# Performance work log

Measured on AMD Instinct MI355X. Metric: run time of the kernel, lower is better.

The kernel has to match this reference:

```python
import jax, jax.numpy as jnp
import numpy as np

N = 10000      # nodes
E = 160000     # edges
G = 64         # graphs
NODE_IN = 115
EDGE_IN = 14
H = 256        # hidden
UH = 64        # EdgeUpdate inner hidden
DEPTH = 5
BN_EPS = 1e-5


def setup_inputs() -> dict:
    key = jax.random.key(0)
    ks = jax.random.split(key, 32)
    p = lambda k, shp: (jax.random.normal(k, shp, dtype=jnp.float32) * 0.05)
    inp = {
        "x": jax.random.normal(ks[0], (N, NODE_IN), dtype=jnp.float32),
        "edge_index": jax.random.randint(ks[1], (2, E), 0, N, dtype=jnp.int64) if jax.config.jax_enable_x64 else jax.random.randint(ks[1], (2, E), 0, N).astype(jnp.int32),
        "edge_attr": jax.random.normal(ks[2], (E, EDGE_IN), dtype=jnp.float32),
        "batch": jnp.sort(jax.random.randint(ks[3], (N,), 0, G)).astype(jnp.int32),
        # projections
        "xp_w": p(ks[4], (NODE_IN, H)), "xp_b": jnp.zeros((H,), jnp.float32),
        "ep_w": p(ks[5], (EDGE_IN, H)), "ep_b": jnp.zeros((H,), jnp.float32),
        # EdgeUpdate MLPs (stacked over depth): Linear(3H -> UH) -> ReLU -> Linear(UH -> H)
        "upd_w1": p(ks[6], (DEPTH, 3 * H, UH)), "upd_b1": jnp.zeros((DEPTH, UH), jnp.float32),
        "upd_w2": p(ks[7], (DEPTH, UH, H)),     "upd_b2": jnp.zeros((DEPTH, H), jnp.float32),
        # GINEConv nn MLPs: Linear(H->H) -> ReLU -> Linear(H->H)
        "conv_w1": p(ks[8], (DEPTH, H, H)), "conv_b1": jnp.zeros((DEPTH, H), jnp.float32),
        "conv_w2": p(ks[9], (DEPTH, H, H)), "conv_b2": jnp.zeros((DEPTH, H), jnp.float32),
        # BatchNorm (eval mode: running stats)
        "bn_g": jnp.ones((DEPTH, H), jnp.float32), "bn_b": jnp.zeros((DEPTH, H), jnp.float32),
        "bn_m": jnp.zeros((DEPTH, H), jnp.float32), "bn_v": jnp.ones((DEPTH, H), jnp.float32),
        # readout
        "ro_w": p(ks[10], (H, H)), "ro_b": jnp.zeros((H,), jnp.float32),
    }
    return inp


def reference(x, edge_index, edge_attr, batch, xp_w, xp_b, ep_w, ep_b,
              upd_w1, upd_b1, upd_w2, upd_b2,
              conv_w1, conv_b1, conv_w2, conv_b2,
              bn_g, bn_b, bn_m, bn_v, ro_w, ro_b):
    src, dst = edge_index[0], edge_index[1]
    x = x @ xp_w + xp_b                       # [N, H]
    e = edge_attr @ ep_w + ep_b               # [E, H]
    for i in range(DEPTH):
        # EdgeUpdate: e = e + MLP([x[src], x[dst], e])
        inp = jnp.concatenate([x[src], x[dst], e], axis=-1)          # [E, 3H]
        h = jax.nn.relu(inp @ upd_w1[i] + upd_b1[i])
        e = e + h @ upd_w2[i] + upd_b2[i]
        # GINEConv (eps=0, edge_dim==hidden -> no edge lin):
        # x_new = mlp(x + sum_{(src->dst)} relu(x[src] + e))
        msg = jax.nn.relu(x[src] + e)                                 # [E, H]
        agg = jax.ops.segment_sum(msg, dst, num_segments=N)           # [N, H]
        z = x + agg
        z = jax.nn.relu(z @ conv_w1[i] + conv_b1[i]) @ conv_w2[i] + conv_b2[i]
        # BatchNorm1d (eval: running stats)
        z = (z - bn_m[i]) * jax.lax.rsqrt(bn_v[i] + BN_EPS) * bn_g[i] + bn_b[i]
        x = x + jax.nn.relu(z)
        # dropout is identity in eval mode
    # global_mean_pool over graphs
    counts = jax.ops.segment_sum(jnp.ones((N,), x.dtype), batch, num_segments=G)
    g = jax.ops.segment_sum(x, batch, num_segments=G) / jnp.maximum(counts, 1.0)[:, None]
    return jax.nn.relu(g @ ro_w + ro_b)       # [G, H]
```

## Files before the change

### kernel.cpp

```cpp
#include <hip/hip_runtime.h>

typedef unsigned short ushort_t;
typedef __attribute__((ext_vector_type(4))) float f32x4;
typedef __attribute__((ext_vector_type(8))) short bf16x8;

constexpr int NN = 10000;
constexpr int NE = 160000;
constexpr int NG = 64;
constexpr int NODE_IN_D = 115;
constexpr int EDGE_IN_D = 14;
constexpr int H = 256;
constexpr int UH = 64;
constexpr int DEPTH_D = 5;
constexpr float BN_EPS_F = 1e-5f;

__device__ __forceinline__ float b2fs(ushort_t u) {
  union { unsigned i; float f; } v; v.i = ((unsigned)u) << 16; return v.f;
}
__device__ __forceinline__ ushort_t f2b(float f) {
  union { float f; unsigned i; } v; v.f = f;
  unsigned x = v.i;
  unsigned r = (x + 0x7fffu + ((x >> 16) & 1u)) >> 16;
  return (ushort_t)r;
}

__global__ __launch_bounds__(256) void k_hist(const int* __restrict__ dst,
                                              int* __restrict__ deg)
{
  int j = blockIdx.x * 256 + threadIdx.x;
  if (j < NE) atomicAdd(&deg[dst[j]], 1);
}

__global__ __launch_bounds__(256) void k_scan(const int* __restrict__ deg,
    int* __restrict__ row_ptr, int* __restrict__ cursor)
{
  __shared__ int part[256];
  const int t = threadIdx.x;
  const int base = t * 40;
  int s = 0;
  for (int i = 0; i < 40; ++i) {
    int idx = base + i;
    if (idx < NN) s += deg[idx];
  }
  part[t] = s;
  __syncthreads();
  for (int off = 1; off < 256; off <<= 1) {
    int v = (t >= off) ? part[t - off] : 0;
    __syncthreads();
    part[t] += v;
    __syncthreads();
  }
  int run = (t > 0) ? part[t - 1] : 0;
  for (int i = 0; i < 40; ++i) {
    int idx = base + i;
    if (idx < NN) {
      row_ptr[idx] = run;
      cursor[idx]  = run;
      run += deg[idx];
    }
  }
  if (t == 255) row_ptr[NN] = NE;
}

__global__ __launch_bounds__(256) void k_scatter(const int* __restrict__ src,
    const int* __restrict__ dst, int* __restrict__ cursor,
    int* __restrict__ perm, int* __restrict__ src_p, int* __restrict__ dst_p)
{
  int j = blockIdx.x * 256 + threadIdx.x;
  if (j < NE) {
    int d = dst[j];
    int pos = atomicAdd(&cursor[d], 1);
    perm[pos] = j;
    src_p[pos] = src[j];
    dst_p[pos] = d;
  }
}

__global__ __launch_bounds__(256) void k_proj_edge(const float* __restrict__ ea,
    const int* __restrict__ perm,
    const float* __restrict__ w, const float* __restrict__ b,
    ushort_t* __restrict__ e_p)
{
  __shared__ float as[16][EDGE_IN_D];
  __shared__ int pj[16];
  const int t = threadIdx.x;
  const int row0 = blockIdx.x * 16;
  if (t < 16) pj[t] = perm[row0 + t];
  __syncthreads();
  if (t < 16 * EDGE_IN_D) {
    int r = t / EDGE_IN_D, c = t - r * EDGE_IN_D;
    as[r][c] = ea[(size_t)pj[r] * EDGE_IN_D + c];
  }
  __syncthreads();
  float acc[16];
#pragma unroll
  for (int m = 0; m < 16; ++m) acc[m] = 0.f;
  for (int k = 0; k < EDGE_IN_D; ++k) {
    float wv = w[(size_t)k * H + t];
#pragma unroll
    for (int m = 0; m < 16; ++m) acc[m] += as[m][k] * wv;
  }
  const float bv = b[t];
  for (int m = 0; m < 16; ++m)
    e_p[(size_t)(row0 + m) * H + t] = f2b(acc[m] + bv);
}

__global__ __launch_bounds__(256) void k_pack_all(
    const float* __restrict__ uw1, const float* __restrict__ uw2,
    const float* __restrict__ cw1, const float* __restrict__ cw2,
    const float* __restrict__ xp_w,
    ushort_t* __restrict__ wcP, ushort_t* __restrict__ w2P,
    ushort_t* __restrict__ c1P, ushort_t* __restrict__ c2P,
    ushort_t* __restrict__ pabP, ushort_t* __restrict__ xpP)
{
  int od = blockIdx.x * 256 + threadIdx.x;
  if (od >= DEPTH_D * 24576) {
    int r = od - DEPTH_D * 24576;
    if (r >= 4096) return;
    int lane = r & 63; int nk = r >> 6;
    int ks = nk & 3, nt = nk >> 2;
    int kbase = ks * 32 + (lane >> 4) * 8;
    int n = nt * 16 + (lane & 15);
    ushort_t v[8];
#pragma unroll
    for (int j = 0; j < 8; ++j) {
      int k = kbase + j;
      v[j] = (k < NODE_IN_D) ? f2b(xp_w[(size_t)k * H + n]) : (ushort_t)0;
    }
    uint4 o;
    o.x = (unsigned)v[0] | ((unsigned)v[1] << 16);
    o.y = (unsigned)v[2] | ((unsigned)v[3] << 16);
    o.z = (unsigned)v[4] | ((unsigned)v[5] << 16);
    o.w = (unsigned)v[6] | ((unsigned)v[7] << 16);
    *(uint4*)(xpP + (size_t)r * 8) = o;
    return;
  }
  int depth = od / 24576;
  int r = od - depth * 24576;
  const float* w1d = uw1 + (size_t)depth * 768 * 64;
  const float* W = nullptr; ushort_t* out = nullptr;
  int N = 0, KS = 8; bool pab = false;
  if (r < 2048)       { W = w1d + 512 * 64; out = wcP + (size_t)depth * 2048 * 8; N = 64; KS = 8; }
  else if (r < 4096)  { r -= 2048;  W = uw2 + (size_t)depth * 64 * 256;  out = w2P + (size_t)depth * 2048 * 8; N = 256; KS = 2; }
  else if (r < 12288) { r -= 4096;  W = cw1 + (size_t)depth * 256 * 256; out = c1P + (size_t)depth * 8192 * 8; N = 256; KS = 8; }
  else if (r < 20480) { r -= 12288; W = cw2 + (size_t)depth * 256 * 256; out = c2P + (size_t)depth * 8192 * 8; N = 256; KS = 8; }
  else                { r -= 20480; out = pabP + (size_t)depth * 4096 * 8; N = 128; KS = 8; pab = true; }
  int lane = r & 63; int nk = r >> 6;
  int ks = nk % KS, nt = nk / KS;
  int kbase = ks * 32 + (lane >> 4) * 8;
  int n = nt * 16 + (lane & 15);
  ushort_t v[8];
#pragma unroll
  for (int j = 0; j < 8; ++j) {
    int k = kbase + j;
    float xv;
    if (!pab) xv = W[(size_t)k * N + n];
    else      xv = (n < 64) ? w1d[(size_t)k * 64 + n]
                            : w1d[(size_t)(256 + k) * 64 + (n - 64)];
    v[j] = f2b(xv);
  }
  uint4 o;
  o.x = (unsigned)v[0] | ((unsigned)v[1] << 16);
  o.y = (unsigned)v[2] | ((unsigned)v[3] << 16);
  o.z = (unsigned)v[4] | ((unsigned)v[5] << 16);
  o.w = (unsigned)v[6] | ((unsigned)v[7] << 16);
  *(uint4*)(out + (size_t)r * 8) = o;
}

__global__ __launch_bounds__(256) void k_projm(const float* __restrict__ x,
    const ushort_t* __restrict__ xpP, const float* __restrict__ xpb,
    const ushort_t* __restrict__ pabP0,
    float* __restrict__ xb, float* __restrict__ Pab)
{
  __shared__ __align__(16) ushort_t sa[2 * 32 * 128];
  __shared__ __align__(16) ushort_t sx[2 * 32 * 256];
  const int t = threadIdx.x, l = t & 63, w = t >> 6;
  const int row0 = blockIdx.x * 32;
#pragma unroll
  for (int it = 0; it < 16; ++it) {
    int idx = t + it * 256;
    int row = idx >> 7, c = idx & 127;
    int grow = row0 + row;
    float v = (grow < NN && c < NODE_IN_D) ? x[(size_t)grow * NODE_IN_D + c] : 0.f;
    ushort_t h = f2b(v);
    ushort_t lo = f2b(v - b2fs(h));
    int sch = (row * 16 + ((c >> 3) ^ (row & 7))) * 8 + (c & 7);
    sa[sch] = h; sa[4096 + sch] = lo;
  }
  __syncthreads();
  const int mt = w & 1, ntb = (w >> 1) * 8;
  const int lrow = l & 15, lhi = l >> 4;
  const int arow = mt * 16 + lrow, sw = arow & 7;
  f32x4 acc[8];
#pragma unroll
  for (int n = 0; n < 8; ++n) acc[n] = (f32x4){0.f, 0.f, 0.f, 0.f};
#pragma unroll
  for (int ks = 0; ks < 4; ++ks) {
    int sch = (arow * 16 + ((ks * 4 + lhi) ^ sw)) * 8;
    bf16x8 ah = *(const bf16x8*)&sa[sch];
    bf16x8 al = *(const bf16x8*)&sa[4096 + sch];
#pragma unroll
    for (int n = 0; n < 8; ++n) {
      bf16x8 bb = *(const bf16x8*)(xpP + (size_t)(((ntb + n) * 4 + ks) * 64 + l) * 8);
      acc[n] = __builtin_amdgcn_mfma_f32_16x16x32_bf16(ah, bb, acc[n], 0, 0, 0);
      acc[n] = __builtin_amdgcn_mfma_f32_16x16x32_bf16(al, bb, acc[n], 0, 0, 0);
    }
  }
#pragma unroll
  for (int n = 0; n < 8; ++n) {
    int col = (ntb + n) * 16 + lrow;
    float bv = xpb[col];
#pragma unroll
    for (int r = 0; r < 4; ++r) {
      int row = mt * 16 + lhi * 4 + r;
      int grow = row0 + row;
      float v = acc[n][r] + bv;
      if (grow < NN) xb[(size_t)grow * H + col] = v;
      ushort_t h = f2b(v);
      ushort_t lo = f2b(v - b2fs(h));
      int sch = (row * 32 + ((col >> 3) ^ (row & 7))) * 8 + (col & 7);
      sx[sch] = h; sx[8192 + sch] = lo;
    }
  }
  __syncthreads();
  const int ntb2 = (w >> 1) * 4;
  f32x4 pacc[4];
#pragma unroll
  for (int n = 0; n < 4; ++n) pacc[n] = (f32x4){0.f, 0.f, 0.f, 0.f};
#pragma unroll
  for (int ks = 0; ks < 8; ++ks) {
    int sch = (arow * 32 + ((ks * 4 + lhi) ^ sw)) * 8;
    bf16x8 ah = *(const bf16x8*)&sx[sch];
    bf16x8 al = *(const bf16x8*)&sx[8192 + sch];
#pragma unroll
    for (int n = 0; n < 4; ++n) {
      bf16x8 bb = *(const bf16x8*)(pabP0 + (size_t)(((ntb2 + n) * 8 + ks) * 64 + l) * 8);
      pacc[n] = __builtin_amdgcn_mfma_f32_16x16x32_bf16(ah, bb, pacc[n], 0, 0, 0);
      pacc[n] = __builtin_amdgcn_mfma_f32_16x16x32_bf16(al, bb, pacc[n], 0, 0, 0);
    }
  }
#pragma unroll
  for (int n = 0; n < 4; ++n) {
    int col = (ntb2 + n) * 16 + lrow;
#pragma unroll
    for (int r = 0; r < 4; ++r) {
      int row = mt * 16 + lhi * 4 + r;
      int grow = row0 + row;
      if (grow < NN) Pab[(size_t)grow * 128 + col] = pacc[n][r];
    }
  }
}

__global__ __launch_bounds__(256) void k_edge_mfma(
    const float* __restrict__ Pab,
    const int* __restrict__ src_p, const int* __restrict__ dst_p,
    const ushort_t* __restrict__ wcP, const float* __restrict__ b1,
    const ushort_t* __restrict__ w2P, const float* __restrict__ b2,
    ushort_t* __restrict__ e_p)
{
  __shared__ __align__(16) ushort_t es[64 * 256];
  __shared__ __align__(16) ushort_t hsm[64 * 64];
  __shared__ int sid[64], did[64];
  const int t = threadIdx.x;
  const int l = t & 63;
  const int w = t >> 6;
  const int e0 = blockIdx.x * 64;
  if (t < 64) { sid[t] = src_p[e0 + t]; did[t] = dst_p[e0 + t]; }
#pragma unroll
  for (int it = 0; it < 8; ++it) {
    int idx = t + it * 256;
    int row = idx >> 5, ch = idx & 31;
    uint4 v = *(const uint4*)(e_p + (size_t)(e0 + row) * H + ch * 8);
    *(uint4*)&es[(row * 32 + (ch ^ (row & 7))) * 8] = v;
  }
  __syncthreads();

  const int rw = w * 16;
  const int lrow = l & 15, lhi = l >> 4;

  bf16x8 af[8];
  {
    int arow = rw + lrow;
    int sw = arow & 7;
#pragma unroll
    for (int ks = 0; ks < 8; ++ks)
      af[ks] = *(const bf16x8*)&es[(arow * 32 + ((ks * 4 + lhi) ^ sw)) * 8];
  }
  f32x4 acc[4];
#pragma unroll
  for (int nt = 0; nt < 4; ++nt) {
    f32x4 a = {0.f, 0.f, 0.f, 0.f};
#pragma unroll
    for (int ks = 0; ks < 8; ++ks) {
      bf16x8 bb = *(const bf16x8*)(wcP + (size_t)((nt * 8 + ks) * 64 + l) * 8);
      a = __builtin_amdgcn_mfma_f32_16x16x32_bf16(af[ks], bb, a, 0, 0, 0);
    }
    acc[nt] = a;
  }
#pragma unroll
  for (int nt = 0; nt < 4; ++nt) {
    int col = nt * 16 + lrow;
    float bv = b1[col];
#pragma unroll
    for (int r = 0; r < 4; ++r) {
      int row = rw + lhi * 4 + r;
      float v = acc[nt][r] + Pab[(size_t)sid[row] * 128 + col]
                           + Pab[(size_t)did[row] * 128 + 64 + col] + bv;
      hsm[row * 64 + (col ^ ((row & 7) << 3))] = f2b(fmaxf(v, 0.f));
    }
  }
  __syncthreads();

  bf16x8 ag[2];
  {
    int arow = rw + lrow;
    int sw = arow & 7;
#pragma unroll
    for (int ks = 0; ks < 2; ++ks)
      ag[ks] = *(const bf16x8*)&hsm[arow * 64 + (((ks * 4 + lhi) ^ sw)) * 8];
  }
#pragma unroll
  for (int nt = 0; nt < 16; ++nt) {
    int col = nt * 16 + lrow;
    float bv = b2[col];
    f32x4 a;
#pragma unroll
    for (int r = 0; r < 4; ++r) {
      int row = rw + lhi * 4 + r;
      a[r] = b2fs(es[row * 256 + (col ^ ((row & 7) << 3))]) + bv;
    }
    bf16x8 bb0 = *(const bf16x8*)(w2P + (size_t)((nt * 2 + 0) * 64 + l) * 8);
    bf16x8 bb1 = *(const bf16x8*)(w2P + (size_t)((nt * 2 + 1) * 64 + l) * 8);
    a = __builtin_amdgcn_mfma_f32_16x16x32_bf16(ag[0], bb0, a, 0, 0, 0);
    a = __builtin_amdgcn_mfma_f32_16x16x32_bf16(ag[1], bb1, a, 0, 0, 0);
#pragma unroll
    for (int r = 0; r < 4; ++r) {
      int row = rw + lhi * 4 + r;
      es[row * 256 + (col ^ ((row & 7) << 3))] = f2b(a[r]);
    }
  }
  __syncthreads();
#pragma unroll
  for (int it = 0; it < 8; ++it) {
    int idx = t + it * 256;
    int row = idx >> 5, ch = idx & 31;
    uint4 v = *(const uint4*)&es[(row * 32 + (ch ^ (row & 7))) * 8];
    *(uint4*)(e_p + (size_t)(e0 + row) * H + ch * 8) = v;
  }
}

__global__ __launch_bounds__(256) void k_agg(
    const ushort_t* __restrict__ e_p, const float* __restrict__ xb,
    const int* __restrict__ src_p, const int* __restrict__ row_ptr,
    float* __restrict__ agg)
{
  const int t = threadIdx.x;
  const int n = blockIdx.x * 4 + (t >> 6);
  const int c0 = (t & 63) * 4;
  const int beg = row_ptr[n], end = row_ptr[n + 1];
  float4 acc = make_float4(0.f, 0.f, 0.f, 0.f);
  for (int j = beg; j < end; ++j) {
    ushort4 ev = *(const ushort4*)(e_p + (size_t)j * H + c0);
    const float4 xv = *(const float4*)(xb + (size_t)src_p[j] * H + c0);
    acc.x += fmaxf(xv.x + b2fs(ev.x), 0.f);
    acc.y += fmaxf(xv.y + b2fs(ev.y), 0.f);
    acc.z += fmaxf(xv.z + b2fs(ev.z), 0.f);
    acc.w += fmaxf(xv.w + b2fs(ev.w), 0.f);
  }
  *(float4*)(agg + (size_t)n * H + c0) = acc;
}

__global__ __launch_bounds__(256) void k_conv1m(const float* __restrict__ xb,
    const float* __restrict__ agg, const ushort_t* __restrict__ wP,
    const float* __restrict__ b, float* __restrict__ t1)
{
  __shared__ __align__(16) ushort_t sm[2 * 16 * 256];
  __shared__ __align__(16) float outs[16 * 256];
  const int t = threadIdx.x, l = t & 63, w = t >> 6;
  const int row0 = blockIdx.x * 16;
#pragma unroll
  for (int it = 0; it < 2; ++it) {
    int idx = t + it * 256;
    int row = idx >> 5, ch = idx & 31;
    int grow = row0 + row;
    float4 p = *(const float4*)(xb + (size_t)grow * H + ch * 8);
    float4 q = *(const float4*)(xb + (size_t)grow * H + ch * 8 + 4);
    float4 g = *(const float4*)(agg + (size_t)grow * H + ch * 8);
    float4 h4 = *(const float4*)(agg + (size_t)grow * H + ch * 8 + 4);
    float v[8] = {p.x + g.x, p.y + g.y, p.z + g.z, p.w + g.w,
                  q.x + h4.x, q.y + h4.y, q.z + h4.z, q.w + h4.w};
    ushort_t h8[8], l8[8];
#pragma unroll
    for (int j = 0; j < 8; ++j) { h8[j] = f2b(v[j]); l8[j] = f2b(v[j] - b2fs(h8[j])); }
    uint4 hh, ll;
    hh.x = (unsigned)h8[0] | ((unsigned)h8[1] << 16);
    hh.y = (unsigned)h8[2] | ((unsigned)h8[3] << 16);
    hh.z = (unsigned)h8[4] | ((unsigned)h8[5] << 16);
    hh.w = (unsigned)h8[6] | ((unsigned)h8[7] << 16);
    ll.x = (unsigned)l8[0] | ((unsigned)l8[1] << 16);
    ll.y = (unsigned)l8[2] | ((unsigned)l8[3] << 16);
    ll.z = (unsigned)l8[4] | ((unsigned)l8[5] << 16);
    ll.w = (unsigned)l8[6] | ((unsigned)l8[7] << 16);
    int sch = (row * 32 + (ch ^ (row & 7))) * 8;
    *(uint4*)&sm[sch] = hh;
    *(uint4*)&sm[4096 + sch] = ll;
  }
  __syncthreads();
  const int lrow = l & 15, lhi = l >> 4;
  const int arow = lrow, sw = arow & 7;
  const int ntb = w * 4;
  f32x4 acc[4];
#pragma unroll
  for (int n = 0; n < 4; ++n) acc[n] = (f32x4){0.f, 0.f, 0.f, 0.f};
#pragma unroll
  for (int ks = 0; ks < 8; ++ks) {
    int sch = (arow * 32 + ((ks * 4 + lhi) ^ sw)) * 8;
    bf16x8 ah = *(const bf16x8*)&sm[sch];
    bf16x8 al = *(const bf16x8*)&sm[4096 + sch];
#pragma unroll
    for (int n = 0; n < 4; ++n) {
      bf16x8 bb = *(const bf16x8*)(wP + (size_t)(((ntb + n) * 8 + ks) * 64 + l) * 8);
      acc[n] = __builtin_amdgcn_mfma_f32_16x16x32_bf16(ah, bb, acc[n], 0, 0, 0);
      acc[n] = __builtin_amdgcn_mfma_f32_16x16x32_bf16(al, bb, acc[n], 0, 0, 0);
    }
  }
#pragma unroll
  for (int n = 0; n < 4; ++n) {
    int col = (ntb + n) * 16 + lrow;
    float bv = b[col];
#pragma unroll
    for (int r = 0; r < 4; ++r)
      outs[(lhi * 4 + r) * 256 + col] = fmaxf(acc[n][r] + bv, 0.f);
  }
  __syncthreads();
#pragma unroll
  for (int it = 0; it < 4; ++it) {
    int idx = t + it * 256;
    int row = idx >> 6, c4 = idx & 63;
    *(float4*)(t1 + (size_t)(row0 + row) * H + c4 * 4) = *(float4*)&outs[row * 256 + c4 * 4];
  }
}

__global__ __launch_bounds__(256) void k_conv2m(const float* __restrict__ t1,
    const ushort_t* __restrict__ wP, const float* __restrict__ cb,
    const float* __restrict__ bng, const float* __restrict__ bnb,
    const float* __restrict__ bnm, const float* __restrict__ bnv,
    float* __restrict__ xb, int do_pab,
    const ushort_t* __restrict__ pabPn, float* __restrict__ Pab)
{
  __shared__ __align__(16) ushort_t sm[2 * 16 * 256];
  __shared__ __align__(16) float outs[16 * 256];
  __shared__ __align__(16) ushort_t sx[2 * 16 * 256];
  const int t = threadIdx.x, l = t & 63, w = t >> 6;
  const int row0 = blockIdx.x * 16;
#pragma unroll
  for (int it = 0; it < 2; ++it) {
    int idx = t + it * 256;
    int row = idx >> 5, ch = idx & 31;
    int grow = row0 + row;
    float4 p = *(const float4*)(t1 + (size_t)grow * H + ch * 8);
    float4 q = *(const float4*)(t1 + (size_t)grow * H + ch * 8 + 4);
    float v[8] = {p.x, p.y, p.z, p.w, q.x, q.y, q.z, q.w};
    ushort_t h8[8], l8[8];
#pragma unroll
    for (int j = 0; j < 8; ++j) { h8[j] = f2b(v[j]); l8[j] = f2b(v[j] - b2fs(h8[j])); }
    uint4 hh, ll;
    hh.x = (unsigned)h8[0] | ((unsigned)h8[1] << 16);
    hh.y = (unsigned)h8[2] | ((unsigned)h8[3] << 16);
    hh.z = (unsigned)h8[4] | ((unsigned)h8[5] << 16);
    hh.w = (unsigned)h8[6] | ((unsigned)h8[7] << 16);
    ll.x = (unsigned)l8[0] | ((unsigned)l8[1] << 16);
    ll.y = (unsigned)l8[2] | ((unsigned)l8[3] << 16);
    ll.z = (unsigned)l8[4] | ((unsigned)l8[5] << 16);
    ll.w = (unsigned)l8[6] | ((unsigned)l8[7] << 16);
    int sch = (row * 32 + (ch ^ (row & 7))) * 8;
    *(uint4*)&sm[sch] = hh;
    *(uint4*)&sm[4096 + sch] = ll;
  }
  __syncthreads();
  const int lrow = l & 15, lhi = l >> 4;
  const int arow = lrow, sw = arow & 7;
  const int ntb = w * 4;
  f32x4 acc[4];
#pragma unroll
  for (int n = 0; n < 4; ++n) acc[n] = (f32x4){0.f, 0.f, 0.f, 0.f};
#pragma unroll
  for (int ks = 0; ks < 8; ++ks) {
    int sch = (arow * 32 + ((ks * 4 + lhi) ^ sw)) * 8;
    bf16x8 ah = *(const bf16x8*)&sm[sch];
    bf16x8 al = *(const bf16x8*)&sm[4096 + sch];
#pragma unroll
    for (int n = 0; n < 4; ++n) {
      bf16x8 bb = *(const bf16x8*)(wP + (size_t)(((ntb + n) * 8 + ks) * 64 + l) * 8);
      acc[n] = __builtin_amdgcn_mfma_f32_16x16x32_bf16(ah, bb, acc[n], 0, 0, 0);
      acc[n] = __builtin_amdgcn_mfma_f32_16x16x32_bf16(al, bb, acc[n], 0, 0, 0);
    }
  }
#pragma unroll
  for (int n = 0; n < 4; ++n) {
    int col = (ntb + n) * 16 + lrow;
    float bv = cb[col];
#pragma unroll
    for (int r = 0; r < 4; ++r)
      outs[(lhi * 4 + r) * 256 + col] = acc[n][r] + bv;
  }
  __syncthreads();
#pragma unroll
  for (int it = 0; it < 4; ++it) {
    int idx = t + it * 256;
    int row = idx >> 6, c4 = idx & 63;
    int grow = row0 + row;
    int c0 = c4 * 4;
    float4 z = *(float4*)&outs[row * 256 + c0];
    float4 g4 = *(const float4*)(bng + c0);
    float4 b4 = *(const float4*)(bnb + c0);
    float4 m4 = *(const float4*)(bnm + c0);
    float4 v4 = *(const float4*)(bnv + c0);
    float4 xv = *(const float4*)(xb + (size_t)grow * H + c0);
    xv.x += fmaxf((z.x - m4.x) * rsqrtf(v4.x + BN_EPS_F) * g4.x + b4.x, 0.f);
    xv.y += fmaxf((z.y - m4.y) * rsqrtf(v4.y + BN_EPS_F) * g4.y + b4.y, 0.f);
    xv.z += fmaxf((z.z - m4.z) * rsqrtf(v4.z + BN_EPS_F) * g4.z + b4.z, 0.f);
    xv.w += fmaxf((z.w - m4.w) * rsqrtf(v4.w + BN_EPS_F) * g4.w + b4.w, 0.f);
    *(float4*)(xb + (size_t)grow * H + c0) = xv;
    if (do_pab) {
      ushort4 hh, ll;
      float vv[4] = {xv.x, xv.y, xv.z, xv.w};
      ushort_t h8[4], l8[4];
#pragma unroll
      for (int j = 0; j < 4; ++j) { h8[j] = f2b(vv[j]); l8[j] = f2b(vv[j] - b2fs(h8[j])); }
      hh.x = h8[0]; hh.y = h8[1]; hh.z = h8[2]; hh.w = h8[3];
      ll.x = l8[0]; ll.y = l8[1]; ll.z = l8[2]; ll.w = l8[3];
      int sch = (row * 32 + ((c0 >> 3) ^ (row & 7))) * 8 + (c0 & 7);
      *(ushort4*)&sx[sch] = hh;
      *(ushort4*)&sx[4096 + sch] = ll;
    }
  }
  if (!do_pab) return;
  __syncthreads();
  const int ntb2 = w * 2;
  f32x4 pacc[2];
#pragma unroll
  for (int n = 0; n < 2; ++n) pacc[n] = (f32x4){0.f, 0.f, 0.f, 0.f};
#pragma unroll
  for (int ks = 0; ks < 8; ++ks) {
    int sch = (arow * 32 + ((ks * 4 + lhi) ^ sw)) * 8;
    bf16x8 ah = *(const bf16x8*)&sx[sch];
    bf16x8 al = *(const bf16x8*)&sx[4096 + sch];
#pragma unroll
    for (int n = 0; n < 2; ++n) {
      bf16x8 bb = *(const bf16x8*)(pabPn + (size_t)(((ntb2 + n) * 8 + ks) * 64 + l) * 8);
      pacc[n] = __builtin_amdgcn_mfma_f32_16x16x32_bf16(ah, bb, pacc[n], 0, 0, 0);
      pacc[n] = __builtin_amdgcn_mfma_f32_16x16x32_bf16(al, bb, pacc[n], 0, 0, 0);
    }
  }
#pragma unroll
  for (int n = 0; n < 2; ++n) {
    int col = (ntb2 + n) * 16 + lrow;
#pragma unroll
    for (int r = 0; r < 4; ++r)
      Pab[(size_t)(row0 + lhi * 4 + r) * 128 + col] = pacc[n][r];
  }
}

__global__ void k_count2(const int* __restrict__ batch, float* __restrict__ gcnt)
{
  int g = threadIdx.x;
  int lo = 0, hi = NN;
  while (lo < hi) { int m = (lo + hi) >> 1; if (batch[m] < g) lo = m + 1; else hi = m; }
  int s = lo;
  lo = 0; hi = NN;
  while (lo < hi) { int m = (lo + hi) >> 1; if (batch[m] <= g) lo = m + 1; else hi = m; }
  gcnt[g] = (float)(lo - s);
}

__global__ __launch_bounds__(256) void k_pool(const float* __restrict__ xb,
    const int* __restrict__ batch, float* __restrict__ gsum)
{
  const int t = threadIdx.x;
  const int row0 = blockIdx.x * 32;
  const int c0 = (t & 63) * 4;
  const int rb = (t >> 6) * 8;
  float4 sum = make_float4(0.f, 0.f, 0.f, 0.f);
  int curg = -1;
#pragma unroll
  for (int j = 0; j < 8; ++j) {
    int row = row0 + rb + j;
    if (row < NN) {
      int g = batch[row];
      if (g != curg) {
        if (curg >= 0) {
          float* gp = gsum + (size_t)curg * H + c0;
          atomicAdd(gp + 0, sum.x); atomicAdd(gp + 1, sum.y);
          atomicAdd(gp + 2, sum.z); atomicAdd(gp + 3, sum.w);
        }
        curg = g;
        sum = make_float4(0.f, 0.f, 0.f, 0.f);
      }
      float4 v = *(const float4*)(xb + (size_t)row * H + c0);
      sum.x += v.x; sum.y += v.y; sum.z += v.z; sum.w += v.w;
    }
  }
  if (curg >= 0) {
    float* gp = gsum + (size_t)curg * H + c0;
    atomicAdd(gp + 0, sum.x); atomicAdd(gp + 1, sum.y);
    atomicAdd(gp + 2, sum.z); atomicAdd(gp + 3, sum.w);
  }
}

__global__ __launch_bounds__(256) void k_readout(const float* __restrict__ gsum,
    const float* __restrict__ gcnt, const float* __restrict__ w,
    const float* __restrict__ b, float* __restrict__ out)
{
  __shared__ float gs[H];
  const int g = blockIdx.x;
  const int t = threadIdx.x;
  float cnt = fmaxf(gcnt[g], 1.0f);
  gs[t] = gsum[(size_t)g * H + t] / cnt;
  __syncthreads();
  float acc = 0.f;
  for (int k = 0; k < H; ++k) acc += gs[k] * w[(size_t)k * H + t];
  out[(size_t)g * H + t] = fmaxf(acc + b[t], 0.f);
}

extern "C" void kernel_launch(void* const* d_in, const int* in_sizes, int n_in,
                              void* d_out, int out_size, void* d_ws, size_t ws_size,
                              hipStream_t stream) {
  (void)in_sizes; (void)n_in; (void)out_size; (void)ws_size;
  const float* x    = (const float*)d_in[0];
  const int*   ei   = (const int*)d_in[1];
  const float* ea   = (const float*)d_in[2];
  const int*   batch= (const int*)d_in[3];
  const float* xp_w = (const float*)d_in[4];
  const float* xp_b = (const float*)d_in[5];
  const float* ep_w = (const float*)d_in[6];
  const float* ep_b = (const float*)d_in[7];
  const float* uw1  = (const float*)d_in[8];
  const float* ub1  = (const float*)d_in[9];
  const float* uw2  = (const float*)d_in[10];
  const float* ub2  = (const float*)d_in[11];
  const float* cw1  = (const float*)d_in[12];
  const float* cb1  = (const float*)d_in[13];
  const float* cw2  = (const float*)d_in[14];
  const float* cb2  = (const float*)d_in[15];
  const float* bng  = (const float*)d_in[16];
  const float* bnb  = (const float*)d_in[17];
  const float* bnm  = (const float*)d_in[18];
  const float* bnv  = (const float*)d_in[19];
  const float* ro_w = (const float*)d_in[20];
  const float* ro_b = (const float*)d_in[21];
  float* out = (float*)d_out;

  char* ws = (char*)d_ws;
  float* xb   = (float*)ws;                  ws += (size_t)NN * H * 4;
  float* agg  = (float*)ws;                  ws += (size_t)NN * H * 4;
  float* t1   = (float*)ws;                  ws += (size_t)NN * H * 4;
  float* Pab  = (float*)ws;                  ws += (size_t)NN * 128 * 4;
  float* gsum = (float*)ws;                  ws += (size_t)NG * H * 4;
  float* gcnt = (float*)ws;                  ws += 256;
  ushort_t* e_p = (ushort_t*)ws;             ws += (size_t)NE * H * 2;
  int* deg    = (int*)ws;                    ws += (size_t)NN * 4;
  int* row_ptr= (int*)ws;                    ws += (size_t)(NN + 8) * 4;
  int* cursor = (int*)ws;                    ws += (size_t)NN * 4;
  int* perm   = (int*)ws;                    ws += (size_t)NE * 4;
  int* src_p  = (int*)ws;                    ws += (size_t)NE * 4;
  int* dst_p  = (int*)ws;                    ws += (size_t)NE * 4;
  ushort_t* wcP = (ushort_t*)ws;             ws += (size_t)DEPTH_D * 2048 * 8 * 2;
  ushort_t* w2P = (ushort_t*)ws;             ws += (size_t)DEPTH_D * 2048 * 8 * 2;
  ushort_t* c1P = (ushort_t*)ws;             ws += (size_t)DEPTH_D * 8192 * 8 * 2;
  ushort_t* c2P = (ushort_t*)ws;             ws += (size_t)DEPTH_D * 8192 * 8 * 2;
  ushort_t* pabP= (ushort_t*)ws;             ws += (size_t)DEPTH_D * 4096 * 8 * 2;
  ushort_t* xpP = (ushort_t*)ws;             ws += (size_t)4096 * 8 * 2;

  const int* src = ei;
  const int* dst = ei + NE;
  const int EB = NE / 256;

  hipMemsetAsync(deg, 0, (size_t)NN * 4, stream);
  k_hist<<<EB, 256, 0, stream>>>(dst, deg);
  k_scan<<<1, 256, 0, stream>>>(deg, row_ptr, cursor);
  k_scatter<<<EB, 256, 0, stream>>>(src, dst, cursor, perm, src_p, dst_p);
  k_pack_all<<<496, 256, 0, stream>>>(uw1, uw2, cw1, cw2, xp_w,
                                      wcP, w2P, c1P, c2P, pabP, xpP);
  k_projm<<<313, 256, 0, stream>>>(x, xpP, xp_b, pabP, xb, Pab);
  k_proj_edge<<<NE / 16, 256, 0, stream>>>(ea, perm, ep_w, ep_b, e_p);

  for (int i = 0; i < DEPTH_D; ++i) {
    k_edge_mfma<<<NE / 64, 256, 0, stream>>>(
        Pab, src_p, dst_p,
        wcP + (size_t)i * 2048 * 8, ub1 + (size_t)i * UH,
        w2P + (size_t)i * 2048 * 8, ub2 + (size_t)i * H,
        e_p);
    k_agg<<<NN / 4, 256, 0, stream>>>(e_p, xb, src_p, row_ptr, agg);
    k_conv1m<<<NN / 16, 256, 0, stream>>>(xb, agg, c1P + (size_t)i * 8192 * 8,
                                          cb1 + (size_t)i * H, t1);
    int do_pab = (i < DEPTH_D - 1) ? 1 : 0;
    k_conv2m<<<NN / 16, 256, 0, stream>>>(t1, c2P + (size_t)i * 8192 * 8,
                                          cb2 + (size_t)i * H,
                                          bng + (size_t)i * H, bnb + (size_t)i * H,
                                          bnm + (size_t)i * H, bnv + (size_t)i * H,
                                          xb, do_pab,
                                          pabP + (size_t)(i + 1 < DEPTH_D ? i + 1 : 0) * 4096 * 8,
                                          Pab);
  }

  hipMemsetAsync(gsum, 0, (size_t)NG * H * 4, stream);
  k_count2<<<1, 64, 0, stream>>>(batch, gcnt);
  k_pool<<<(NN + 31) / 32, 256, 0, stream>>>(xb, batch, gsum);
  k_readout<<<NG, 256, 0, stream>>>(gsum, gcnt, ro_w, ro_b, out);
}
```

Measured before the change: 662.6 us.

## Fuse edge aggregation into edge-update kernel and merge both conv MLP kernels

The dst-sorted segment sum moves into the edge MLP kernel. Each wave accumulates relu(x[src]+e) over runs of equal dst in its 16 edges and flushes to agg with fp32 atomics, so the separate k_agg pass no longer re-reads the updated edge tensor. The two GINE MLP GEMM kernels become one, keeping the hidden activation in shared memory as hi/lo bf16 instead of a global t1 buffer. The final layer also skips writing the edge tensor back. The cost is a per-layer memset of agg, atomic contention, non-deterministic summation order, and higher shared-memory use in the fused conv kernel.

```diff
diff --git a/kernel.cpp b/kernel.cpp
--- a/kernel.cpp
+++ b/kernel.cpp
@@ -256,7 +256,8 @@
     const int* __restrict__ src_p, const int* __restrict__ dst_p,
     const ushort_t* __restrict__ wcP, const float* __restrict__ b1,
     const ushort_t* __restrict__ w2P, const float* __restrict__ b2,
-    ushort_t* __restrict__ e_p)
+    ushort_t* __restrict__ e_p,
+    const float* __restrict__ xb, float* __restrict__ agg, int write_e)
 {
   __shared__ __align__(16) ushort_t es[64 * 256];
   __shared__ __align__(16) ushort_t hsm[64 * 64];
@@ -340,41 +341,56 @@
     }
   }
   __syncthreads();
-#pragma unroll
-  for (int it = 0; it < 8; ++it) {
-    int idx = t + it * 256;
-    int row = idx >> 5, ch = idx & 31;
-    uint4 v = *(const uint4*)&es[(row * 32 + (ch ^ (row & 7))) * 8];
-    *(uint4*)(e_p + (size_t)(e0 + row) * H + ch * 8) = v;
-  }
-}
-
-__global__ __launch_bounds__(256) void k_agg(
-    const ushort_t* __restrict__ e_p, const float* __restrict__ xb,
-    const int* __restrict__ src_p, const int* __restrict__ row_ptr,
-    float* __restrict__ agg)
-{
-  const int t = threadIdx.x;
-  const int n = blockIdx.x * 4 + (t >> 6);
-  const int c0 = (t & 63) * 4;
-  const int beg = row_ptr[n], end = row_ptr[n + 1];
-  float4 acc = make_float4(0.f, 0.f, 0.f, 0.f);
-  for (int j = beg; j < end; ++j) {
-    ushort4 ev = *(const ushort4*)(e_p + (size_t)j * H + c0);
-    const float4 xv = *(const float4*)(xb + (size_t)src_p[j] * H + c0);
-    acc.x += fmaxf(xv.x + b2fs(ev.x), 0.f);
-    acc.y += fmaxf(xv.y + b2fs(ev.y), 0.f);
-    acc.z += fmaxf(xv.z + b2fs(ev.z), 0.f);
-    acc.w += fmaxf(xv.w + b2fs(ev.w), 0.f);
-  }
-  *(float4*)(agg + (size_t)n * H + c0) = acc;
-}
-
-__global__ __launch_bounds__(256) void k_conv1m(const float* __restrict__ xb,
-    const float* __restrict__ agg, const ushort_t* __restrict__ wP,
-    const float* __restrict__ b, float* __restrict__ t1)
+
+  if (write_e) {
+#pragma unroll
+    for (int it = 0; it < 8; ++it) {
+      int idx = t + it * 256;
+      int row = idx >> 5, ch = idx & 31;
+      uint4 v = *(const uint4*)&es[(row * 32 + (ch ^ (row & 7))) * 8];
+      *(uint4*)(e_p + (size_t)(e0 + row) * H + ch * 8) = v;
+    }
+  }
+
+  {
+    const int c0 = l * 4;
+    float4 acc4 = make_float4(0.f, 0.f, 0.f, 0.f);
+    int cur = did[rw];
+#pragma unroll
+    for (int r = 0; r < 16; ++r) {
+      int row = rw + r;
+      int d = did[row];
+      if (d != cur) {
+        float* gp = agg + (size_t)cur * H + c0;
+        atomicAdd(gp + 0, acc4.x); atomicAdd(gp + 1, acc4.y);
+        atomicAdd(gp + 2, acc4.z); atomicAdd(gp + 3, acc4.w);
+        acc4 = make_float4(0.f, 0.f, 0.f, 0.f);
+        cur = d;
+      }
+      ushort4 ev = *(const ushort4*)&es[row * 256 + (c0 ^ ((row & 7) << 3))];
+      float4 xv = *(const float4*)(xb + (size_t)sid[row] * H + c0);
+      acc4.x += fmaxf(xv.x + b2fs(ev.x), 0.f);
+      acc4.y += fmaxf(xv.y + b2fs(ev.y), 0.f);
+      acc4.z += fmaxf(xv.z + b2fs(ev.z), 0.f);
+      acc4.w += fmaxf(xv.w + b2fs(ev.w), 0.f);
+    }
+    float* gp = agg + (size_t)cur * H + c0;
+    atomicAdd(gp + 0, acc4.x); atomicAdd(gp + 1, acc4.y);
+    atomicAdd(gp + 2, acc4.z); atomicAdd(gp + 3, acc4.w);
+  }
+}
+
+__global__ __launch_bounds__(256) void k_convm(
+    const float* __restrict__ agg,
+    const ushort_t* __restrict__ w1P, const float* __restrict__ b1v,
+    const ushort_t* __restrict__ w2P, const float* __restrict__ cb2v,
+    const float* __restrict__ bng, const float* __restrict__ bnb,
+    const float* __restrict__ bnm, const float* __restrict__ bnv,
+    float* __restrict__ xb, int do_pab,
+    const ushort_t* __restrict__ pabPn, float* __restrict__ Pab)
 {
   __shared__ __align__(16) ushort_t sm[2 * 16 * 256];
+  __shared__ __align__(16) ushort_t st1[2 * 16 * 256];
   __shared__ __align__(16) float outs[16 * 256];
   const int t = threadIdx.x, l = t & 63, w = t >> 6;
   const int row0 = blockIdx.x * 16;
@@ -419,7 +435,7 @@
     bf16x8 al = *(const bf16x8*)&sm[4096 + sch];
 #pragma unroll
     for (int n = 0; n < 4; ++n) {
-      bf16x8 bb = *(const bf16x8*)(wP + (size_t)(((ntb + n) * 8 + ks) * 64 + l) * 8);
+      bf16x8 bb = *(const bf16x8*)(w1P + (size_t)(((ntb + n) * 8 + ks) * 64 + l) * 8);
       acc[n] = __builtin_amdgcn_mfma_f32_16x16x32_bf16(ah, bb, acc[n], 0, 0, 0);
       acc[n] = __builtin_amdgcn_mfma_f32_16x16x32_bf16(al, bb, acc[n], 0, 0, 0);
     }
@@ -427,82 +443,40 @@
 #pragma unroll
   for (int n = 0; n < 4; ++n) {
     int col = (ntb + n) * 16 + lrow;
-    float bv = b[col];
-#pragma unroll
-    for (int r = 0; r < 4; ++r)
-      outs[(lhi * 4 + r) * 256 + col] = fmaxf(acc[n][r] + bv, 0.f);
-  }
-  __syncthreads();
-#pragma unroll
-  for (int it = 0; it < 4; ++it) {
-    int idx = t + it * 256;
-    int row = idx >> 6, c4 = idx & 63;
-    *(float4*)(t1 + (size_t)(row0 + row) * H + c4 * 4) = *(float4*)&outs[row * 256 + c4 * 4];
-  }
-}
-
-__global__ __launch_bounds__(256) void k_conv2m(const float* __restrict__ t1,
-    const ushort_t* __restrict__ wP, const float* __restrict__ cb,
-    const float* __restrict__ bng, const float* __restrict__ bnb,
-    const float* __restrict__ bnm, const float* __restrict__ bnv,
-    float* __restrict__ xb, int do_pab,
-    const ushort_t* __restrict__ pabPn, float* __restrict__ Pab)
-{
-  __shared__ __align__(16) ushort_t sm[2 * 16 * 256];
-  __shared__ __align__(16) float outs[16 * 256];
-  __shared__ __align__(16) ushort_t sx[2 * 16 * 256];
-  const int t = threadIdx.x, l = t & 63, w = t >> 6;
-  const int row0 = blockIdx.x * 16;
-#pragma unroll
-  for (int it = 0; it < 2; ++it) {
-    int idx = t + it * 256;
-    int row = idx >> 5, ch = idx & 31;
-    int grow = row0 + row;
-    float4 p = *(const float4*)(t1 + (size_t)grow * H + ch * 8);
-    float4 q = *(const float4*)(t1 + (size_t)grow * H + ch * 8 + 4);
-    float v[8] = {p.x, p.y, p.z, p.w, q.x, q.y, q.z, q.w};
-    ushort_t h8[8], l8[8];
-#pragma unroll
-    for (int j = 0; j < 8; ++j) { h8[j] = f2b(v[j]); l8[j] = f2b(v[j] - b2fs(h8[j])); }
-    uint4 hh, ll;
-    hh.x = (unsigned)h8[0] | ((unsigned)h8[1] << 16);
-    hh.y = (unsigned)h8[2] | ((unsigned)h8[3] << 16);
-    hh.z = (unsigned)h8[4] | ((unsigned)h8[5] << 16);
-    hh.w = (unsigned)h8[6] | ((unsigned)h8[7] << 16);
-    ll.x = (unsigned)l8[0] | ((unsigned)l8[1] << 16);
-    ll.y = (unsigned)l8[2] | ((unsigned)l8[3] << 16);
-    ll.z = (unsigned)l8[4] | ((unsigned)l8[5] << 16);
-    ll.w = (unsigned)l8[6] | ((unsigned)l8[7] << 16);
-    int sch = (row * 32 + (ch ^ (row & 7))) * 8;
-    *(uint4*)&sm[sch] = hh;
-    *(uint4*)&sm[4096 + sch] = ll;
-  }
-  __syncthreads();
-  const int lrow = l & 15, lhi = l >> 4;
-  const int arow = lrow, sw = arow & 7;
-  const int ntb = w * 4;
-  f32x4 acc[4];
-#pragma unroll
-  for (int n = 0; n < 4; ++n) acc[n] = (f32x4){0.f, 0.f, 0.f, 0.f};
+    float bv = b1v[col];
+#pragma unroll
+    for (int r = 0; r < 4; ++r) {
+      int row = lhi * 4 + r;
+      float v = fmaxf(acc[n][r] + bv, 0.f);
+      ushort_t h = f2b(v);
+      ushort_t lo = f2b(v - b2fs(h));
+      int sch = (row * 32 + ((col >> 3) ^ (row & 7))) * 8 + (col & 7);
+      st1[sch] = h; st1[4096 + sch] = lo;
+    }
+  }
+  __syncthreads();
+  f32x4 acc2[4];
+#pragma unroll
+  for (int n = 0; n < 4; ++n) acc2[n] = (f32x4){0.f, 0.f, 0.f, 0.f};
 #pragma unroll
   for (int ks = 0; ks < 8; ++ks) {
     int sch = (arow * 32 + ((ks * 4 + lhi) ^ sw)) * 8;
-    bf16x8 ah = *(const bf16x8*)&sm[sch];
-    bf16x8 al = *(const bf16x8*)&sm[4096 + sch];
+    bf16x8 ah = *(const bf16x8*)&st1[sch];
+    bf16x8 al = *(const bf16x8*)&st1[4096 + sch];
 #pragma unroll
     for (int n = 0; n < 4; ++n) {
-      bf16x8 bb = *(const bf16x8*)(wP + (size_t)(((ntb + n) * 8 + ks) * 64 + l) * 8);
-      acc[n] = __builtin_amdgcn_mfma_f32_16x16x32_bf16(ah, bb, acc[n], 0, 0, 0);
-      acc[n] = __builtin_amdgcn_mfma_f32_16x16x32_bf16(al, bb, acc[n], 0, 0, 0);
+      bf16x8 bb = *(const bf16x8*)(w2P + (size_t)(((ntb + n) * 8 + ks) * 64 + l) * 8);
+      acc2[n] = __builtin_amdgcn_mfma_f32_16x16x32_bf16(ah, bb, acc2[n], 0, 0, 0);
+      acc2[n] = __builtin_amdgcn_mfma_f32_16x16x32_bf16(al, bb, acc2[n], 0, 0, 0);
     }
   }
 #pragma unroll
   for (int n = 0; n < 4; ++n) {
     int col = (ntb + n) * 16 + lrow;
-    float bv = cb[col];
+    float bv = cb2v[col];
 #pragma unroll
     for (int r = 0; r < 4; ++r)
-      outs[(lhi * 4 + r) * 256 + col] = acc[n][r] + bv;
+      outs[(lhi * 4 + r) * 256 + col] = acc2[n][r] + bv;
   }
   __syncthreads();
 #pragma unroll
@@ -523,16 +497,16 @@
     xv.w += fmaxf((z.w - m4.w) * rsqrtf(v4.w + BN_EPS_F) * g4.w + b4.w, 0.f);
     *(float4*)(xb + (size_t)grow * H + c0) = xv;
     if (do_pab) {
-      ushort4 hh, ll;
       float vv[4] = {xv.x, xv.y, xv.z, xv.w};
       ushort_t h8[4], l8[4];
 #pragma unroll
       for (int j = 0; j < 4; ++j) { h8[j] = f2b(vv[j]); l8[j] = f2b(vv[j] - b2fs(h8[j])); }
+      ushort4 hh, ll;
       hh.x = h8[0]; hh.y = h8[1]; hh.z = h8[2]; hh.w = h8[3];
       ll.x = l8[0]; ll.y = l8[1]; ll.z = l8[2]; ll.w = l8[3];
       int sch = (row * 32 + ((c0 >> 3) ^ (row & 7))) * 8 + (c0 & 7);
-      *(ushort4*)&sx[sch] = hh;
-      *(ushort4*)&sx[4096 + sch] = ll;
+      *(ushort4*)&sm[sch] = hh;
+      *(ushort4*)&sm[4096 + sch] = ll;
     }
   }
   if (!do_pab) return;
@@ -544,8 +518,8 @@
 #pragma unroll
   for (int ks = 0; ks < 8; ++ks) {
     int sch = (arow * 32 + ((ks * 4 + lhi) ^ sw)) * 8;
-    bf16x8 ah = *(const bf16x8*)&sx[sch];
-    bf16x8 al = *(const bf16x8*)&sx[4096 + sch];
+    bf16x8 ah = *(const bf16x8*)&sm[sch];
+    bf16x8 al = *(const bf16x8*)&sm[4096 + sch];
 #pragma unroll
     for (int n = 0; n < 2; ++n) {
       bf16x8 bb = *(const bf16x8*)(pabPn + (size_t)(((ntb2 + n) * 8 + ks) * 64 + l) * 8);
@@ -653,7 +627,6 @@
   char* ws = (char*)d_ws;
   float* xb   = (float*)ws;                  ws += (size_t)NN * H * 4;
   float* agg  = (float*)ws;                  ws += (size_t)NN * H * 4;
-  float* t1   = (float*)ws;                  ws += (size_t)NN * H * 4;
   float* Pab  = (float*)ws;                  ws += (size_t)NN * 128 * 4;
   float* gsum = (float*)ws;                  ws += (size_t)NG * H * 4;
   float* gcnt = (float*)ws;                  ws += 256;
@@ -685,22 +658,23 @@
   k_proj_edge<<<NE / 16, 256, 0, stream>>>(ea, perm, ep_w, ep_b, e_p);
 
   for (int i = 0; i < DEPTH_D; ++i) {
+    hipMemsetAsync(agg, 0, (size_t)NN * H * 4, stream);
+    int write_e = (i < DEPTH_D - 1) ? 1 : 0;
     k_edge_mfma<<<NE / 64, 256, 0, stream>>>(
         Pab, src_p, dst_p,
         wcP + (size_t)i * 2048 * 8, ub1 + (size_t)i * UH,
         w2P + (size_t)i * 2048 * 8, ub2 + (size_t)i * H,
-        e_p);
-    k_agg<<<NN / 4, 256, 0, stream>>>(e_p, xb, src_p, row_ptr, agg);
-    k_conv1m<<<NN / 16, 256, 0, stream>>>(xb, agg, c1P + (size_t)i * 8192 * 8,
-                                          cb1 + (size_t)i * H, t1);
+        e_p, xb, agg, write_e);
     int do_pab = (i < DEPTH_D - 1) ? 1 : 0;
-    k_conv2m<<<NN / 16, 256, 0, stream>>>(t1, c2P + (size_t)i * 8192 * 8,
-                                          cb2 + (size_t)i * H,
-                                          bng + (size_t)i * H, bnb + (size_t)i * H,
-                                          bnm + (size_t)i * H, bnv + (size_t)i * H,
-                                          xb, do_pab,
-                                          pabP + (size_t)(i + 1 < DEPTH_D ? i + 1 : 0) * 4096 * 8,
-                                          Pab);
+    k_convm<<<NN / 16, 256, 0, stream>>>(
+        agg,
+        c1P + (size_t)i * 8192 * 8, cb1 + (size_t)i * H,
+        c2P + (size_t)i * 8192 * 8, cb2 + (size_t)i * H,
+        bng + (size_t)i * H, bnb + (size_t)i * H,
+        bnm + (size_t)i * H, bnv + (size_t)i * H,
+        xb, do_pab,
+        pabP + (size_t)(i + 1 < DEPTH_D ? i + 1 : 0) * 4096 * 8,
+        Pab);
   }
 
   hipMemsetAsync(gsum, 0, (size_t)NG * H * 4, stream);
```

Result: slower. 739.2 us (+11.6%).
